# Kernel tuning notes

Measured on AMD Instinct MI355X. Metric: run time of the kernel, lower is better.

## Reference

```python
import jax, jax.numpy as jnp
import numpy as np

B, N, M = 32, 32, 64          # batch, timesteps, local group length (group_token_length+3)
NL, NG = 192, 768             # n_embd_local, n_embd_global
HL, HG = 6, 12                # n_head_local, n_head_global


def setup_inputs() -> dict:
    key = jax.random.key(0)
    ks = jax.random.split(key, 16)
    def w(k, shape, s=0.02):
        return jax.random.normal(k, shape, jnp.float32) * s
    inp = {}
    inp["xl"] = jax.random.normal(ks[0], (B, N, M, NL), jnp.float32)
    inp["xg"] = jax.random.normal(ks[1], (B, 2 * N, NG), jnp.float32)
    i = 2
    for pre, d in (("l", NL), ("g", NG)):
        inp[f"{pre}_ln1_w"] = jnp.ones((d,), jnp.float32)
        inp[f"{pre}_ln1_b"] = jnp.zeros((d,), jnp.float32)
        inp[f"{pre}_ln2_w"] = jnp.ones((d,), jnp.float32)
        inp[f"{pre}_ln2_b"] = jnp.zeros((d,), jnp.float32)
        for nm in ("q", "k", "v", "o"):
            inp[f"{pre}_w{nm}"] = w(ks[i], (d, d)); i += 1
            inp[f"{pre}_b{nm}"] = jnp.zeros((d,), jnp.float32)
        inp[f"{pre}_w1"] = w(ks[i], (d, 4 * d)); i += 1
        inp[f"{pre}_b1"] = jnp.zeros((4 * d,), jnp.float32)
        inp[f"{pre}_w2"] = w(ks[i], (4 * d, d)); i += 1
        inp[f"{pre}_b2"] = jnp.zeros((d,), jnp.float32)
    inp["d_w"] = w(ks[i], (M * NL, NG))
    inp["d_b"] = jnp.zeros((NG,), jnp.float32)
    return inp


def _ln(x, g, b):
    m = x.mean(-1, keepdims=True)
    v = ((x - m) ** 2).mean(-1, keepdims=True)
    return (x - m) / jnp.sqrt(v + 1e-5) * g + b


def _attn(x, wq, bq, wk, bk, wv, bv, wo, bo, nh, allow):
    # x: [B', L, D]; allow: [L, L] bool (True = attend)
    Bx, L, D = x.shape
    hd = D // nh
    q = (x @ wq + bq).reshape(Bx, L, nh, hd)
    k = (x @ wk + bk).reshape(Bx, L, nh, hd)
    v = (x @ wv + bv).reshape(Bx, L, nh, hd)
    s = jnp.einsum('bihd,bjhd->bhij', q, k) / np.float32(np.sqrt(hd))
    s = jnp.where(allow[None, None], s, -jnp.inf)
    p = jax.nn.softmax(s, axis=-1)
    y = jnp.einsum('bhij,bjhd->bihd', p, v).reshape(Bx, L, D)
    return y @ wo + bo


def _tblock(x, p, nh, allow):
    (ln1w, ln1b, ln2w, ln2b, wq, bq, wk, bk, wv, bv, wo, bo, w1, b1, w2, b2) = p
    x = x + _attn(_ln(x, ln1w, ln1b), wq, bq, wk, bk, wv, bv, wo, bo, nh, allow)
    h = _ln(x, ln2w, ln2b)
    return x + (jax.nn.gelu(h @ w1 + b1, approximate=False) @ w2 + b2)


def reference(xl, xg,
              l_ln1_w, l_ln1_b, l_ln2_w, l_ln2_b,
              l_wq, l_bq, l_wk, l_bk, l_wv, l_bv, l_wo, l_bo,
              l_w1, l_b1, l_w2, l_b2,
              g_ln1_w, g_ln1_b, g_ln2_w, g_ln2_b,
              g_wq, g_bq, g_wk, g_bk, g_wv, g_bv, g_wo, g_bo,
              g_w1, g_b1, g_w2, g_b2,
              d_w, d_b):
    Bx, Nx, Mx, nl = xl.shape
    ng = xg.shape[-1]
    lp = (l_ln1_w, l_ln1_b, l_ln2_w, l_ln2_b, l_wq, l_bq, l_wk, l_bk,
          l_wv, l_bv, l_wo, l_bo, l_w1, l_b1, l_w2, l_b2)
    gp = (g_ln1_w, g_ln1_b, g_ln2_w, g_ln2_b, g_wq, g_bq, g_wk, g_bk,
          g_wv, g_bv, g_wo, g_bo, g_w1, g_b1, g_w2, g_b2)

    # local block: causal attention within each group of M tokens
    allow_l = jnp.tril(jnp.ones((Mx, Mx), bool))
    x = _tblock(xl.reshape(Bx * Nx, Mx, nl), lp, HL, allow_l)
    xl_out = x.reshape(Bx, Nx, Mx, nl)

    # summarize each group into one global token, interleave with xg pairs
    zg = (xl_out.reshape(Bx, Nx, Mx * nl) @ d_w + d_b)[:, :, None, :]  # [B,N,1,ng]
    zg = jnp.concatenate([zg, xg.reshape(Bx, Nx, 2, ng)], axis=2)      # [B,N,3,ng]
    zg = zg.reshape(Bx, 3 * Nx, ng)

    # global mask: tril plus within-triplet upper entries; the global block
    # additionally applies its own causal mask, so combined = causal & custom
    L = 3 * Nx
    idx = jnp.arange(L)
    causal = idx[:, None] >= idx[None, :]
    custom = causal | (idx[:, None] // 3 == idx[None, :] // 3)
    allow_g = causal & custom

    zg = _tblock(zg, gp, HG, allow_g)
    xg_out = zg.reshape(Bx, Nx, 3, ng)[:, :, 1:, :].reshape(Bx, 2 * Nx, ng)
    return (xl_out, xg_out)
```

## Files before the change

### kernel.cpp

```cpp
#include <hip/hip_runtime.h>
#include <hip/hip_bf16.h>


typedef unsigned short ushort;
typedef __bf16 bf16x8 __attribute__((ext_vector_type(8)));
typedef float f32x4 __attribute__((ext_vector_type(4)));

__device__ __forceinline__ ushort f2us(float f) {
  __hip_bfloat16 h = __float2bfloat16(f);
  return *reinterpret_cast<ushort*>(&h);
}
__device__ __forceinline__ float gelu_exact(float v) {
  return 0.5f * v * (1.f + erff(v * 0.70710678118654752f));
}
__device__ __forceinline__ void gload16(const ushort* g, ushort* l) {
  __builtin_amdgcn_global_load_lds(
      (const __attribute__((address_space(1))) void*)g,
      (__attribute__((address_space(3))) void*)l, 16, 0, 0);
}

struct TJobs { const float* s[13]; ushort* d[13]; };

__global__ __launch_bounds__(256)
void transp_all(TJobs J)
{
  static constexpr int NN[13]  = {192,192,192,192,768,192,768,768,768,768,768,3072,768};
  static constexpr int SS[13]  = {192,192,192,192,192,768,12288,768,768,768,768,768,3072};
  static constexpr int RO[13]  = {0,192,384,0,0,0,0,0,768,1536,0,0,0};
  static constexpr int CUM[14] = {0,9,18,27,36,72,108,2412,2556,2700,2844,2988,3564,4140};
  __shared__ float t[64][65];
  int bid = blockIdx.x;
  int j = 0;
  while (bid >= CUM[j + 1]) ++j;
  int tIdx = bid - CUM[j];
  const int N = NN[j], stride = SS[j], rowOff = RO[j];
  const int nx = N >> 6;
  const int n0 = (tIdx % nx) * 64, k0 = (tIdx / nx) * 64;
  const float* W = J.s[j];
  ushort* Wt = J.d[j];
  int c = threadIdx.x & 63, r = threadIdx.x >> 6;
  #pragma unroll
  for (int i = 0; i < 16; ++i) {
    int kr = r + i * 4;
    t[kr][c] = W[(size_t)(k0 + kr) * N + n0 + c];
  }
  __syncthreads();
  #pragma unroll
  for (int i = 0; i < 16; ++i) {
    int nr = r + i * 4;
    Wt[(size_t)(rowOff + n0 + nr) * stride + k0 + c] = f2us(t[c][nr]);
  }
}

__global__ __launch_bounds__(256)
void pack3_kernel(float* dst, const float* a, int na, const float* b, int nb,
                  const float* c, int nc)
{
  int i = blockIdx.x * 256 + threadIdx.x;
  if (i >= na + nb + nc) return;
  dst[i] = (i < na) ? a[i] : (i < na + nb ? b[i - na] : c[i - na - nb]);
}

template<int D>
__global__ __launch_bounds__(256)
void ln_kernel(const float* __restrict__ x, const float* __restrict__ g,
               const float* __restrict__ bb, ushort* __restrict__ out, int rows)
{
  int wave = threadIdx.x >> 6, lane = threadIdx.x & 63;
  int row = blockIdx.x * 4 + wave;
  if (row >= rows) return;
  const float* xr = x + (size_t)row * D;
  constexpr int E = D / 64;
  float vals[E];
  float s = 0.f;
  #pragma unroll
  for (int e = 0; e < E; ++e) { vals[e] = xr[e * 64 + lane]; s += vals[e]; }
  #pragma unroll
  for (int off = 32; off >= 1; off >>= 1) s += __shfl_xor(s, off);
  float m = s * (1.f / D);
  float s2 = 0.f;
  #pragma unroll
  for (int e = 0; e < E; ++e) { float d = vals[e] - m; s2 += d * d; }
  #pragma unroll
  for (int off = 32; off >= 1; off >>= 1) s2 += __shfl_xor(s2, off);
  float rstd = rsqrtf(s2 * (1.f / D) + 1e-5f);
  ushort* orow = out + (size_t)row * D;
  #pragma unroll
  for (int e = 0; e < E; ++e) {
    int c = e * 64 + lane;
    orow[c] = f2us((vals[e] - m) * rstd * g[c] + bb[c]);
  }
}

__global__ __launch_bounds__(256, 2)
void fused_mlp(const ushort* __restrict__ A, const ushort* __restrict__ W1t,
               const ushort* __restrict__ W2t, const float* __restrict__ b1,
               const float* __restrict__ b2, const float* __restrict__ resF,
               float* __restrict__ Cf, ushort* __restrict__ Cb)
{
  __shared__ __align__(16) ushort W1B[64 * 200];
  __shared__ __align__(16) ushort W2B[192 * 72];
  __shared__ __align__(16) ushort Hs[64 * 72];
  const int tid = threadIdx.x;
  const int wave = tid >> 6, lane = tid & 63;
  const int quad = lane >> 4, lm = lane & 15;
  const int rowBase = blockIdx.x * 64;
  const int wr  = (wave & 1) * 32;
  const int wc1 = (wave >> 1) * 32;
  const int wc2 = (wave >> 1) * 96;

  bf16x8 afr[2][6];
  #pragma unroll
  for (int r2 = 0; r2 < 2; ++r2)
    #pragma unroll
    for (int kt = 0; kt < 6; ++kt)
      afr[r2][kt] = *reinterpret_cast<const bf16x8*>(
          &A[(size_t)(rowBase + wr + r2 * 16 + lm) * 192 + kt * 32 + quad * 8]);

  uint4 rs1[6], rs2[6];
  #pragma unroll
  for (int i = 0; i < 6; ++i) {
    int seg = tid + i * 256, row = seg / 24, kk = (seg % 24) * 8;
    rs1[i] = *reinterpret_cast<const uint4*>(&W1t[(size_t)row * 192 + kk]);
  }
  #pragma unroll
  for (int i = 0; i < 6; ++i) {
    int seg = tid + i * 256, row = seg / 24, kk = (seg % 24) * 8;
    *reinterpret_cast<uint4*>(&W1B[row * 200 + kk]) = rs1[i];
  }
  #pragma unroll
  for (int i = 0; i < 6; ++i) {
    int seg = tid + i * 256, row = seg / 8, kk = (seg % 8) * 8;
    rs2[i] = *reinterpret_cast<const uint4*>(&W2t[(size_t)row * 768 + kk]);
  }
  __syncthreads();

  f32x4 acc2[2][6] = {};
  for (int ht = 0; ht < 12; ++ht) {
    f32x4 acc1[2][2] = {};
    #pragma unroll
    for (int kt = 0; kt < 6; ++kt) {
      bf16x8 bfr[2];
      #pragma unroll
      for (int c2 = 0; c2 < 2; ++c2)
        bfr[c2] = *reinterpret_cast<const bf16x8*>(
            &W1B[(wc1 + c2 * 16 + lm) * 200 + kt * 32 + quad * 8]);
      #pragma unroll
      for (int r2 = 0; r2 < 2; ++r2)
        #pragma unroll
        for (int c2 = 0; c2 < 2; ++c2)
          acc1[r2][c2] = __builtin_amdgcn_mfma_f32_16x16x32_bf16(
              afr[r2][kt], bfr[c2], acc1[r2][c2], 0, 0, 0);
    }
    #pragma unroll
    for (int r2 = 0; r2 < 2; ++r2)
      #pragma unroll
      for (int c2 = 0; c2 < 2; ++c2) {
        int col = wc1 + c2 * 16 + lm;
        float bb1 = b1[ht * 64 + col];
        #pragma unroll
        for (int g = 0; g < 4; ++g) {
          int row = wr + r2 * 16 + quad * 4 + g;
          Hs[row * 72 + col] = f2us(gelu_exact(acc1[r2][c2][g] + bb1));
        }
      }
    #pragma unroll
    for (int i = 0; i < 6; ++i) {
      int seg = tid + i * 256, row = seg / 8, kk = (seg % 8) * 8;
      *reinterpret_cast<uint4*>(&W2B[row * 72 + kk]) = rs2[i];
    }
    if (ht + 1 < 12) {
      #pragma unroll
      for (int i = 0; i < 6; ++i) {
        int seg = tid + i * 256, row = seg / 24, kk = (seg % 24) * 8;
        rs1[i] = *reinterpret_cast<const uint4*>(
            &W1t[(size_t)((ht + 1) * 64 + row) * 192 + kk]);
      }
    }
    __syncthreads();
    #pragma unroll
    for (int s = 0; s < 2; ++s) {
      bf16x8 ap[2], bp[6];
      #pragma unroll
      for (int r2 = 0; r2 < 2; ++r2)
        ap[r2] = *reinterpret_cast<const bf16x8*>(
            &Hs[(wr + r2 * 16 + lm) * 72 + s * 32 + quad * 8]);
      #pragma unroll
      for (int c2 = 0; c2 < 6; ++c2)
        bp[c2] = *reinterpret_cast<const bf16x8*>(
            &W2B[(wc2 + c2 * 16 + lm) * 72 + s * 32 + quad * 8]);
      #pragma unroll
      for (int r2 = 0; r2 < 2; ++r2)
        #pragma unroll
        for (int c2 = 0; c2 < 6; ++c2)
          acc2[r2][c2] = __builtin_amdgcn_mfma_f32_16x16x32_bf16(
              ap[r2], bp[c2], acc2[r2][c2], 0, 0, 0);
    }
    if (ht + 1 < 12) {
      #pragma unroll
      for (int i = 0; i < 6; ++i) {
        int seg = tid + i * 256, row = seg / 24, kk = (seg % 24) * 8;
        *reinterpret_cast<uint4*>(&W1B[row * 200 + kk]) = rs1[i];
      }
      #pragma unroll
      for (int i = 0; i < 6; ++i) {
        int seg = tid + i * 256, row = seg / 8, kk = (seg % 8) * 8;
        rs2[i] = *reinterpret_cast<const uint4*>(
            &W2t[(size_t)row * 768 + (ht + 1) * 64 + kk]);
      }
      __syncthreads();
    }
  }
  #pragma unroll
  for (int r2 = 0; r2 < 2; ++r2)
    #pragma unroll
    for (int c2 = 0; c2 < 6; ++c2) {
      int col = wc2 + c2 * 16 + lm;
      float bb2 = b2[col];
      #pragma unroll
      for (int g = 0; g < 4; ++g) {
        int row = rowBase + wr + r2 * 16 + quad * 4 + g;
        size_t idx = (size_t)row * 192 + col;
        float v = acc2[r2][c2][g] + bb2 + resF[idx];
        Cf[idx] = v;
        Cb[idx] = f2us(v);
      }
    }
}

template<int ACT, int RES, int OUTF, int OUTB, int BIAS>
__global__ __launch_bounds__(256)
void mgemm(const ushort* __restrict__ A, const ushort* __restrict__ Bt,
           const float* __restrict__ bias, const float* __restrict__ resF,
           float* __restrict__ Cf, ushort* __restrict__ Cb,
           int M, int N, int K)
{
  __shared__ __align__(16) ushort Asm[2][128 * 32];
  __shared__ __align__(16) ushort Bsm[2][64 * 32];
  const int tid = threadIdx.x;
  const int wave = tid >> 6, lane = tid & 63;
  const int quad = lane >> 4, lm = lane & 15;
  const int rowBase = blockIdx.y * 128, colBase = blockIdx.x * 64;
  const int wrow = (wave & 1) * 64, wcol = (wave >> 1) * 32;
  const int srow = lane >> 2, skcol = (lane & 3) * 8;
  const int nIter = K >> 5;

  auto stage = [&](int buf, int it) {
    const int k0 = it * 32;
    #pragma unroll
    for (int uu = 0; uu < 3; ++uu) {
      const int u = wave * 3 + uu;
      if (u < 8) {
        const ushort* gp = A + (size_t)(rowBase + u * 16 + srow) * K + k0 + skcol;
        gload16(gp, &Asm[buf][u * 512]);
      } else {
        const int v = u - 8;
        const ushort* gp = Bt + (size_t)(colBase + v * 16 + srow) * K + k0 + skcol;
        gload16(gp, &Bsm[buf][v * 512]);
      }
    }
  };

  f32x4 acc[4][2] = {};
  stage(0, 0);
  if (nIter > 1) stage(1, 1);

  for (int t = 0; t < nIter; ++t) {
    const int cur = t & 1;
    if (t + 1 < nIter) asm volatile("s_waitcnt vmcnt(3)" ::: "memory");
    else               asm volatile("s_waitcnt vmcnt(0)" ::: "memory");
    __builtin_amdgcn_s_barrier();
    bf16x8 af[4], bfr[2];
    #pragma unroll
    for (int r2 = 0; r2 < 4; ++r2)
      af[r2] = *reinterpret_cast<const bf16x8*>(&Asm[cur][(wrow + r2 * 16 + lm) * 32 + quad * 8]);
    #pragma unroll
    for (int c2 = 0; c2 < 2; ++c2)
      bfr[c2] = *reinterpret_cast<const bf16x8*>(&Bsm[cur][(wcol + c2 * 16 + lm) * 32 + quad * 8]);
    asm volatile("s_waitcnt lgkmcnt(0)" ::: "memory");
    __builtin_amdgcn_s_barrier();
    if (t + 2 < nIter) stage(cur, t + 2);
    #pragma unroll
    for (int r2 = 0; r2 < 4; ++r2)
      #pragma unroll
      for (int c2 = 0; c2 < 2; ++c2)
        acc[r2][c2] = __builtin_amdgcn_mfma_f32_16x16x32_bf16(af[r2], bfr[c2], acc[r2][c2], 0, 0, 0);
  }

  #pragma unroll
  for (int r2 = 0; r2 < 4; ++r2) {
    #pragma unroll
    for (int c2 = 0; c2 < 2; ++c2) {
      int col = colBase + wcol + c2 * 16 + lm;
      int row0 = rowBase + wrow + r2 * 16 + quad * 4;
      #pragma unroll
      for (int g = 0; g < 4; ++g) {
        float v = acc[r2][c2][g];
        size_t idx = (size_t)(row0 + g) * N + col;
        if (BIAS) v += bias[col];
        if (ACT == 1) v = gelu_exact(v);
        if (RES) v += resF[idx];
        if (OUTF) Cf[idx] = v;
        if (OUTB) Cb[idx] = f2us(v);
      }
    }
  }
}

template<int ACT, int RES, int OUTF, int OUTB, int BIAS, int SPLITK>
__global__ __launch_bounds__(256)
void mgemm128(const ushort* __restrict__ A, const ushort* __restrict__ Bt,
              const float* __restrict__ bias, const float* __restrict__ resF,
              float* __restrict__ Cf, ushort* __restrict__ Cb,
              int M, int N, int K, int kChunk)
{
  __shared__ __align__(16) ushort Asm[2][128 * 32];
  __shared__ __align__(16) ushort Bsm[2][128 * 32];
  const int tid = threadIdx.x;
  const int wave = tid >> 6, lane = tid & 63;
  const int quad = lane >> 4, lm = lane & 15;
  const int rowBase = blockIdx.y * 128, colBase = blockIdx.x * 128;
  const int wrow = (wave & 1) * 64, wcol = (wave >> 1) * 64;
  const int srow = lane >> 2, skcol = (lane & 3) * 8;

  const int kbeg = SPLITK ? blockIdx.z * kChunk : 0;
  const int nIter = (SPLITK ? kChunk : K) >> 5;

  auto stage = [&](int buf, int it) {
    const int k0 = kbeg + it * 32;
    #pragma unroll
    for (int uu = 0; uu < 4; ++uu) {
      const int u = wave * 4 + uu;
      if (u < 8) {
        const ushort* gp = A + (size_t)(rowBase + u * 16 + srow) * K + k0 + skcol;
        gload16(gp, &Asm[buf][u * 512]);
      } else {
        const int v = u - 8;
        const ushort* gp = Bt + (size_t)(colBase + v * 16 + srow) * K + k0 + skcol;
        gload16(gp, &Bsm[buf][v * 512]);
      }
    }
  };

  f32x4 acc[4][4] = {};
  stage(0, 0);
  if (nIter > 1) stage(1, 1);

  for (int t = 0; t < nIter; ++t) {
    const int cur = t & 1;
    if (t + 1 < nIter) asm volatile("s_waitcnt vmcnt(4)" ::: "memory");
    else               asm volatile("s_waitcnt vmcnt(0)" ::: "memory");
    __builtin_amdgcn_s_barrier();
    bf16x8 af[4], bfr[4];
    #pragma unroll
    for (int r2 = 0; r2 < 4; ++r2)
      af[r2] = *reinterpret_cast<const bf16x8*>(&Asm[cur][(wrow + r2 * 16 + lm) * 32 + quad * 8]);
    #pragma unroll
    for (int c2 = 0; c2 < 4; ++c2)
      bfr[c2] = *reinterpret_cast<const bf16x8*>(&Bsm[cur][(wcol + c2 * 16 + lm) * 32 + quad * 8]);
    asm volatile("s_waitcnt lgkmcnt(0)" ::: "memory");
    __builtin_amdgcn_s_barrier();
    if (t + 2 < nIter) stage(cur, t + 2);
    #pragma unroll
    for (int r2 = 0; r2 < 4; ++r2)
      #pragma unroll
      for (int c2 = 0; c2 < 4; ++c2)
        acc[r2][c2] = __builtin_amdgcn_mfma_f32_16x16x32_bf16(af[r2], bfr[c2], acc[r2][c2], 0, 0, 0);
  }

  const size_t zoff = SPLITK ? (size_t)blockIdx.z * M * N : 0;
  #pragma unroll
  for (int r2 = 0; r2 < 4; ++r2) {
    #pragma unroll
    for (int c2 = 0; c2 < 4; ++c2) {
      int col = colBase + wcol + c2 * 16 + lm;
      int row0 = rowBase + wrow + r2 * 16 + quad * 4;
      #pragma unroll
      for (int g = 0; g < 4; ++g) {
        float v = acc[r2][c2][g];
        size_t idx = (size_t)(row0 + g) * N + col;
        if (BIAS) v += bias[col];
        if (ACT == 1) v = gelu_exact(v);
        if (RES) v += resF[idx];
        if (OUTF) Cf[zoff + idx] = v;
        if (OUTB) Cb[idx] = f2us(v);
      }
    }
  }
}

__global__ __launch_bounds__(256)
void reduce8_kernel(const float* __restrict__ P, const float* __restrict__ db,
                    float* __restrict__ ZG)
{
  int i = blockIdx.x * 256 + threadIdx.x;
  float s = db[i % 768];
  #pragma unroll
  for (int k = 0; k < 8; ++k) s += P[i + k * 786432];
  ZG[i] = s;
}

__global__ __launch_bounds__(256)
void reduce4res_kernel(const float* __restrict__ P, const float* __restrict__ db,
                       const float* __restrict__ res, float* __restrict__ out)
{
  int i = blockIdx.x * 256 + threadIdx.x;
  float s = db[i % 768] + res[i];
  #pragma unroll
  for (int k = 0; k < 4; ++k) s += P[i + k * 2359296];
  out[i] = s;
}

template<int L, int HD, int NW>
__global__ __launch_bounds__(NW * 64)
void fattn(const ushort* __restrict__ QKV, ushort* __restrict__ Yp,
           int nh, int DS, int DY, int offQ, int offK, int offV)
{
  constexpr int PQ = HD + 8;
  constexpr int PV = L + 8;
  constexpr int KS = HD / 32;
  constexpr int NCT = L / 16;
  constexpr int KS2 = L / 32;
  constexpr int NYT = HD / 16;
  constexpr int T = NW * 64;
  __shared__ __align__(16) ushort Ql[L * PQ];
  __shared__ __align__(16) ushort Kl[L * PQ];
  __shared__ __align__(16) ushort Vt[HD * PV];
  __shared__ __align__(16) ushort Ps[L * PV];
  const int tid = threadIdx.x;
  const int b = blockIdx.x / nh, h = blockIdx.x % nh;
  const size_t rowb = (size_t)b * L * DS;
  const int hb = h * HD;
  constexpr int CH = L * HD / 8;
  for (int idx = tid; idx < CH; idx += T) {
    int row = idx / (HD / 8), seg = idx % (HD / 8);
    uint4 q4 = *reinterpret_cast<const uint4*>(&QKV[rowb + (size_t)row * DS + offQ + hb + seg * 8]);
    *reinterpret_cast<uint4*>(&Ql[row * PQ + seg * 8]) = q4;
    uint4 k4 = *reinterpret_cast<const uint4*>(&QKV[rowb + (size_t)row * DS + offK + hb + seg * 8]);
    *reinterpret_cast<uint4*>(&Kl[row * PQ + seg * 8]) = k4;
  }
  for (int idx = tid; idx < L * HD; idx += T) {
    int j = idx / HD, d = idx % HD;
    Vt[d * PV + j] = QKV[rowb + (size_t)j * DS + offV + hb + d];
  }
  __syncthreads();
  const int lane = tid & 63;
  const int quad = lane >> 4, lm = lane & 15;
  const int rt = tid >> 6;
  const float scale = rsqrtf((float)HD);
  bf16x8 af[KS];
  #pragma unroll
  for (int s = 0; s < KS; ++s)
    af[s] = *reinterpret_cast<const bf16x8*>(&Ql[(rt * 16 + lm) * PQ + s * 32 + quad * 8]);
  f32x4 sacc[NCT] = {};
  #pragma unroll
  for (int ct = 0; ct < NCT; ++ct)
    #pragma unroll
    for (int s = 0; s < KS; ++s) {
      bf16x8 bf = *reinterpret_cast<const bf16x8*>(&Kl[(ct * 16 + lm) * PQ + s * 32 + quad * 8]);
      sacc[ct] = __builtin_amdgcn_mfma_f32_16x16x32_bf16(af[s], bf, sacc[ct], 0, 0, 0);
    }
  float inv[4];
  #pragma unroll
  for (int g = 0; g < 4; ++g) {
    const int row = rt * 16 + quad * 4 + g;
    float sv[NCT]; float m = -1e30f;
    #pragma unroll
    for (int ct = 0; ct < NCT; ++ct) {
      int col = ct * 16 + lm;
      float x = sacc[ct][g] * scale;
      sv[ct] = (col <= row) ? x : -1e30f;
      m = fmaxf(m, sv[ct]);
    }
    #pragma unroll
    for (int off = 8; off >= 1; off >>= 1) m = fmaxf(m, __shfl_xor(m, off));
    float l = 0.f;
    #pragma unroll
    for (int ct = 0; ct < NCT; ++ct) {
      float p = __expf(sv[ct] - m);
      l += p;
      Ps[row * PV + ct * 16 + lm] = f2us(p);
    }
    #pragma unroll
    for (int off = 8; off >= 1; off >>= 1) l += __shfl_xor(l, off);
    inv[g] = 1.f / l;
  }
  __syncthreads();
  f32x4 yacc[NYT] = {};
  #pragma unroll
  for (int s = 0; s < KS2; ++s) {
    bf16x8 ap = *reinterpret_cast<const bf16x8*>(&Ps[(rt * 16 + lm) * PV + s * 32 + quad * 8]);
    #pragma unroll
    for (int ct = 0; ct < NYT; ++ct) {
      bf16x8 bv = *reinterpret_cast<const bf16x8*>(&Vt[(ct * 16 + lm) * PV + s * 32 + quad * 8]);
      yacc[ct] = __builtin_amdgcn_mfma_f32_16x16x32_bf16(ap, bv, yacc[ct], 0, 0, 0);
    }
  }
  #pragma unroll
  for (int ct = 0; ct < NYT; ++ct)
    #pragma unroll
    for (int g = 0; g < 4; ++g) {
      int row = rt * 16 + quad * 4 + g;
      int d = ct * 16 + lm;
      Yp[((size_t)b * L + row) * DY + hb + d] = f2us(yacc[ct][g] * inv[g]);
    }
}

__global__ __launch_bounds__(256)
void interleave_kernel(const float* __restrict__ zg, const float* __restrict__ xg,
                       float* __restrict__ z)
{
  int idx = blockIdx.x * 256 + threadIdx.x;
  int c = idx % 768;
  int tok = idx / 768;
  int b = tok / 96, r = tok % 96;
  int n = r / 3, t = r % 3;
  z[idx] = (t == 0) ? zg[((size_t)b * 32 + n) * 768 + c]
                    : xg[((size_t)b * 64 + 2 * n + (t - 1)) * 768 + c];
}

__global__ __launch_bounds__(256)
void gather_kernel(const float* __restrict__ zfin, float* __restrict__ dst)
{
  int idx = blockIdx.x * 256 + threadIdx.x;
  int c = idx % 768;
  int t = (idx / 768) % 64;
  int b = idx / (768 * 64);
  int n = t >> 1, s = t & 1;
  dst[idx] = zfin[((size_t)b * 96 + 3 * n + 1 + s) * 768 + c];
}

extern "C" void kernel_launch(void* const* d_in, const int* in_sizes, int n_in,
                              void* d_out, int out_size, void* d_ws, size_t ws_size,
                              hipStream_t stream) {
  const float* xl = (const float*)d_in[0];
  const float* xg = (const float*)d_in[1];
  const float* l_ln1_w = (const float*)d_in[2];  const float* l_ln1_b = (const float*)d_in[3];
  const float* l_ln2_w = (const float*)d_in[4];  const float* l_ln2_b = (const float*)d_in[5];
  const float* l_wq = (const float*)d_in[6];     const float* l_bq = (const float*)d_in[7];
  const float* l_wk = (const float*)d_in[8];     const float* l_bk = (const float*)d_in[9];
  const float* l_wv = (const float*)d_in[10];    const float* l_bv = (const float*)d_in[11];
  const float* l_wo = (const float*)d_in[12];    const float* l_bo = (const float*)d_in[13];
  const float* l_w1 = (const float*)d_in[14];    const float* l_b1 = (const float*)d_in[15];
  const float* l_w2 = (const float*)d_in[16];    const float* l_b2 = (const float*)d_in[17];
  const float* g_ln1_w = (const float*)d_in[18]; const float* g_ln1_b = (const float*)d_in[19];
  const float* g_ln2_w = (const float*)d_in[20]; const float* g_ln2_b = (const float*)d_in[21];
  const float* g_wq = (const float*)d_in[22];    const float* g_bq = (const float*)d_in[23];
  const float* g_wk = (const float*)d_in[24];    const float* g_bk = (const float*)d_in[25];
  const float* g_wv = (const float*)d_in[26];    const float* g_bv = (const float*)d_in[27];
  const float* g_wo = (const float*)d_in[28];    const float* g_bo = (const float*)d_in[29];
  const float* g_w1 = (const float*)d_in[30];    const float* g_b1 = (const float*)d_in[31];
  const float* g_w2 = (const float*)d_in[32];    const float* g_b2 = (const float*)d_in[33];
  const float* dw   = (const float*)d_in[34];    const float* db   = (const float*)d_in[35];

  float* outL = (float*)d_out;
  float* outG = outL + 12582912;

  char* W = (char*)d_ws;
  ushort* A_bf   = (ushort*)(W + 0);
  ushort* QKVl   = (ushort*)(W + 25165824);
  ushort* XLb    = (ushort*)(W + 75497472);
  float*  X1     = (float*)(W + 100663296);
  ushort* wqkv_t = (ushort*)(W + 150994944);
  ushort* wo_t   = (ushort*)(W + 151216128);
  ushort* w1_t   = (ushort*)(W + 151289856);
  ushort* w2_t   = (ushort*)(W + 151584768);
  ushort* wd_t   = (ushort*)(W + 151879680);
  ushort* wgqkv_t= (ushort*)(W + 170754048);
  ushort* wgo_t  = (ushort*)(W + 174292992);
  ushort* wg1_t  = (ushort*)(W + 175472640);
  ushort* wg2_t  = (ushort*)(W + 180191232);
  float*  bqkv_l = (float*)(W + 184909824);
  float*  bqkv_g = (float*)(W + 184912128);
  float*  ZGP  = (float*)(W + 0);
  float*  FC2P = (float*)(W + 0);
  float*  ZG   = (float*)(W + 25165824);
  float*  Z    = (float*)(W + 28311552);
  ushort* LNG  = (ushort*)(W + 37748736);
  ushort* QKVg = (ushort*)(W + 42467328);
  ushort* YG   = (ushort*)(W + 56623104);
  float*  X1G  = (float*)(W + 61341696);
  ushort* HLNG = (ushort*)(W + 70778880);
  ushort* HIDg = (ushort*)(W + 100663296);
  float*  OUTG = (float*)(W + 119537664);

  TJobs tj;
  tj.s[0] = l_wq; tj.s[1] = l_wk; tj.s[2] = l_wv; tj.s[3] = l_wo;
  tj.s[4] = l_w1; tj.s[5] = l_w2; tj.s[6] = dw;
  tj.s[7] = g_wq; tj.s[8] = g_wk; tj.s[9] = g_wv; tj.s[10] = g_wo;
  tj.s[11] = g_w1; tj.s[12] = g_w2;
  tj.d[0] = wqkv_t; tj.d[1] = wqkv_t; tj.d[2] = wqkv_t; tj.d[3] = wo_t;
  tj.d[4] = w1_t; tj.d[5] = w2_t; tj.d[6] = wd_t;
  tj.d[7] = wgqkv_t; tj.d[8] = wgqkv_t; tj.d[9] = wgqkv_t; tj.d[10] = wgo_t;
  tj.d[11] = wg1_t; tj.d[12] = wg2_t;
  transp_all<<<4140, 256, 0, stream>>>(tj);
  pack3_kernel<<<3, 256, 0, stream>>>(bqkv_l, l_bq, 192, l_bk, 192, l_bv, 192);
  pack3_kernel<<<9, 256, 0, stream>>>(bqkv_g, g_bq, 768, g_bk, 768, g_bv, 768);

  ln_kernel<192><<<16384, 256, 0, stream>>>(xl, l_ln1_w, l_ln1_b, A_bf, 65536);
  mgemm<0,0,0,1,1><<<dim3(9,512), 256, 0, stream>>>(A_bf, wqkv_t, bqkv_l, nullptr, nullptr, QKVl, 65536, 576, 192);
  fattn<64,32,4><<<6144, 256, 0, stream>>>(QKVl, A_bf, 6, 576, 192, 0, 192, 384);
  mgemm<0,1,1,0,1><<<dim3(3,512), 256, 0, stream>>>(A_bf, wo_t, l_bo, xl, X1, nullptr, 65536, 192, 192);
  ln_kernel<192><<<16384, 256, 0, stream>>>(X1, l_ln2_w, l_ln2_b, A_bf, 65536);
  fused_mlp<<<1024, 256, 0, stream>>>(A_bf, w1_t, w2_t, l_b1, l_b2, X1, outL, XLb);
  mgemm128<0,0,1,0,0,1><<<dim3(6,8,8), 256, 0, stream>>>(XLb, wd_t, nullptr, nullptr, ZGP, nullptr, 1024, 768, 12288, 1536);
  reduce8_kernel<<<3072, 256, 0, stream>>>(ZGP, db, ZG);
  interleave_kernel<<<9216, 256, 0, stream>>>(ZG, xg, Z);
  ln_kernel<768><<<768, 256, 0, stream>>>(Z, g_ln1_w, g_ln1_b, LNG, 3072);
  mgemm128<0,0,0,1,1,0><<<dim3(18,24), 256, 0, stream>>>(LNG, wgqkv_t, bqkv_g, nullptr, nullptr, QKVg, 3072, 2304, 768, 0);
  fattn<96,64,6><<<384, 384, 0, stream>>>(QKVg, YG, 12, 2304, 768, 0, 768, 1536);
  mgemm<0,1,1,0,1><<<dim3(12,24), 256, 0, stream>>>(YG, wgo_t, g_bo, Z, X1G, nullptr, 3072, 768, 768);
  ln_kernel<768><<<768, 256, 0, stream>>>(X1G, g_ln2_w, g_ln2_b, HLNG, 3072);
  mgemm128<1,0,0,1,1,0><<<dim3(24,24), 256, 0, stream>>>(HLNG, wg1_t, g_b1, nullptr, nullptr, HIDg, 3072, 3072, 768, 0);
  mgemm128<0,0,1,0,0,1><<<dim3(6,24,4), 256, 0, stream>>>(HIDg, wg2_t, nullptr, nullptr, FC2P, nullptr, 3072, 768, 3072, 768);
  reduce4res_kernel<<<9216, 256, 0, stream>>>(FC2P, g_b2, X1G, OUTG);
  gather_kernel<<<6144, 256, 0, stream>>>(OUTG, outG);
}
```

Baseline: 750.5 us.

## Read MLP weight fragments directly from global memory instead of LDS staging

The fused local MLP kernel no longer stages W1 and W2 tiles through shared memory with register prefetch. Each wave now loads its MFMA B-operand fragments straight from global memory, relying on L2/L1 caching since every block reads the same weights. This removes the LDS copies and cuts shared memory use, which may allow more resident blocks. In exchange, weight reads become redundant across waves and are no longer overlapped with compute through prefetch. An extra barrier is added to protect the reuse of the Hs tile.

```diff
diff --git a/kernel.cpp b/kernel.cpp
--- a/kernel.cpp
+++ b/kernel.cpp
@@ -98,8 +98,6 @@
                const float* __restrict__ b2, const float* __restrict__ resF,
                float* __restrict__ Cf, ushort* __restrict__ Cb)
 {
-  __shared__ __align__(16) ushort W1B[64 * 200];
-  __shared__ __align__(16) ushort W2B[192 * 72];
   __shared__ __align__(16) ushort Hs[64 * 72];
   const int tid = threadIdx.x;
   const int wave = tid >> 6, lane = tid & 63;
@@ -117,24 +115,6 @@
       afr[r2][kt] = *reinterpret_cast<const bf16x8*>(
           &A[(size_t)(rowBase + wr + r2 * 16 + lm) * 192 + kt * 32 + quad * 8]);
 
-  uint4 rs1[6], rs2[6];
-  #pragma unroll
-  for (int i = 0; i < 6; ++i) {
-    int seg = tid + i * 256, row = seg / 24, kk = (seg % 24) * 8;
-    rs1[i] = *reinterpret_cast<const uint4*>(&W1t[(size_t)row * 192 + kk]);
-  }
-  #pragma unroll
-  for (int i = 0; i < 6; ++i) {
-    int seg = tid + i * 256, row = seg / 24, kk = (seg % 24) * 8;
-    *reinterpret_cast<uint4*>(&W1B[row * 200 + kk]) = rs1[i];
-  }
-  #pragma unroll
-  for (int i = 0; i < 6; ++i) {
-    int seg = tid + i * 256, row = seg / 8, kk = (seg % 8) * 8;
-    rs2[i] = *reinterpret_cast<const uint4*>(&W2t[(size_t)row * 768 + kk]);
-  }
-  __syncthreads();
-
   f32x4 acc2[2][6] = {};
   for (int ht = 0; ht < 12; ++ht) {
     f32x4 acc1[2][2] = {};
@@ -144,7 +124,7 @@
       #pragma unroll
       for (int c2 = 0; c2 < 2; ++c2)
         bfr[c2] = *reinterpret_cast<const bf16x8*>(
-            &W1B[(wc1 + c2 * 16 + lm) * 200 + kt * 32 + quad * 8]);
+            &W1t[(size_t)(ht * 64 + wc1 + c2 * 16 + lm) * 192 + kt * 32 + quad * 8]);
       #pragma unroll
       for (int r2 = 0; r2 < 2; ++r2)
         #pragma unroll
@@ -152,6 +132,7 @@
           acc1[r2][c2] = __builtin_amdgcn_mfma_f32_16x16x32_bf16(
               afr[r2][kt], bfr[c2], acc1[r2][c2], 0, 0, 0);
     }
+    __syncthreads();
     #pragma unroll
     for (int r2 = 0; r2 < 2; ++r2)
       #pragma unroll
@@ -164,19 +145,6 @@
           Hs[row * 72 + col] = f2us(gelu_exact(acc1[r2][c2][g] + bb1));
         }
       }
-    #pragma unroll
-    for (int i = 0; i < 6; ++i) {
-      int seg = tid + i * 256, row = seg / 8, kk = (seg % 8) * 8;
-      *reinterpret_cast<uint4*>(&W2B[row * 72 + kk]) = rs2[i];
-    }
-    if (ht + 1 < 12) {
-      #pragma unroll
-      for (int i = 0; i < 6; ++i) {
-        int seg = tid + i * 256, row = seg / 24, kk = (seg % 24) * 8;
-        rs1[i] = *reinterpret_cast<const uint4*>(
-            &W1t[(size_t)((ht + 1) * 64 + row) * 192 + kk]);
-      }
-    }
     __syncthreads();
     #pragma unroll
     for (int s = 0; s < 2; ++s) {
@@ -188,27 +156,13 @@
       #pragma unroll
       for (int c2 = 0; c2 < 6; ++c2)
         bp[c2] = *reinterpret_cast<const bf16x8*>(
-            &W2B[(wc2 + c2 * 16 + lm) * 72 + s * 32 + quad * 8]);
+            &W2t[(size_t)(wc2 + c2 * 16 + lm) * 768 + ht * 64 + s * 32 + quad * 8]);
       #pragma unroll
       for (int r2 = 0; r2 < 2; ++r2)
         #pragma unroll
         for (int c2 = 0; c2 < 6; ++c2)
           acc2[r2][c2] = __builtin_amdgcn_mfma_f32_16x16x32_bf16(
               ap[r2], bp[c2], acc2[r2][c2], 0, 0, 0);
-    }
-    if (ht + 1 < 12) {
-      #pragma unroll
-      for (int i = 0; i < 6; ++i) {
-        int seg = tid + i * 256, row = seg / 24, kk = (seg % 24) * 8;
-        *reinterpret_cast<uint4*>(&W1B[row * 200 + kk]) = rs1[i];
-      }
-      #pragma unroll
-      for (int i = 0; i < 6; ++i) {
-        int seg = tid + i * 256, row = seg / 8, kk = (seg % 8) * 8;
-        rs2[i] = *reinterpret_cast<const uint4*>(
-            &W2t[(size_t)row * 768 + (ht + 1) * 64 + kk]);
-      }
-      __syncthreads();
     }
   }
   #pragma unroll
```

After: 699.0 us. 6.9% less time.
